# Kernel tuning notes

Measured on AMD Instinct MI355X. Metric: run time of the kernel, lower is better.

The kernel has to match this reference:

```python
import jax, jax.numpy as jnp
import numpy as np

BATCH = 64
IN_VECN = 1024
IN_VECL = 64
OUT_VECN = 64
OUT_VECL = 32
ROUTINGS = 3
EPS = 1e-5


def squash(x, axis=-1, eps=EPS):
    # squash(x) = |x|^2/(1+|x|^2) * x/(|x|+eps), matching the torch source
    n = jnp.linalg.norm(x, axis=axis, keepdims=True)
    n2 = n * n
    return n2 / (1.0 + n2) * x / (n + eps)


def setup_inputs() -> dict:
    key = jax.random.key(0)
    k1, k2, k3 = jax.random.split(key, 3)
    stdv = 1.0 / np.sqrt(IN_VECN * IN_VECL)  # reset_parameters: uniform(-stdv, stdv)
    u = jax.random.normal(k1, (BATCH, IN_VECN, IN_VECL), dtype=jnp.float32)
    weight = jax.random.uniform(k2, (IN_VECN, OUT_VECN, OUT_VECL, IN_VECL),
                                dtype=jnp.float32, minval=-stdv, maxval=stdv)
    bias = jax.random.uniform(k3, (IN_VECN, OUT_VECN, OUT_VECL),
                              dtype=jnp.float32, minval=-stdv, maxval=stdv)
    return {"u": u, "weight": weight, "bias": bias}


def reference(u, weight, bias):
    # u: [B, N, I]; weight: [N, O, L, I]; bias: [N, O, L]
    # u_hat: [B, N, O, L] -- per-input-capsule prediction for each output capsule
    u_hat = jnp.einsum('bni,noli->bnol', u, weight) + bias[None]
    # retain_grad=False: routing uses detached u_hat
    ud = jax.lax.stop_gradient(u_hat)
    # initial c = softmax(zeros) over out_vecn -> uniform 1/O, shape [1,1,O,1]
    c = jnp.full((1, 1, OUT_VECN, 1), 1.0 / OUT_VECN, dtype=u.dtype)
    b = jnp.zeros((u.shape[0], IN_VECN, OUT_VECN, 1), dtype=u.dtype)
    for _ in range(ROUTINGS - 1):
        v = squash(jnp.sum(ud * c, axis=-3), axis=-1)        # [B, O, L]
        b = b + jnp.sum(ud * v[:, None], axis=-1, keepdims=True)  # [B, N, O, 1]
        c = jax.nn.softmax(b, axis=-2)                        # softmax over O
    return squash(jnp.sum(u_hat * c, axis=-3), axis=-1)      # [B, O, L]
```

## Files before the change

### kernel.cpp

```cpp
#include <hip/hip_runtime.h>

#define BATCH 64
#define NIN 1024
#define IVL 64
#define ONUM 64
#define LVL 32
#define OLSZ 2048

typedef __attribute__((ext_vector_type(4))) float f32x4;
typedef __attribute__((ext_vector_type(8))) short short8;

#define STR_(x) #x
#define STR(x) STR_(x)

static __device__ __forceinline__ unsigned short f2bf(float f) {
  unsigned u = __builtin_bit_cast(unsigned, f);
  u += 0x7fffu + ((u >> 16) & 1u);
  return (unsigned short)(u >> 16);
}
static __device__ __forceinline__ float bf2f_lo(unsigned x) {
  return __builtin_bit_cast(float, x << 16);
}
static __device__ __forceinline__ float bf2f_hi(unsigned x) {
  return __builtin_bit_cast(float, x & 0xffff0000u);
}

#define W_BURST8(W, q0, q1)                                              \
  asm volatile(                                                          \
      "global_load_dwordx4 %[w0], %[a0], off\n\t"                        \
      "global_load_dwordx4 %[w1], %[a0], off offset:16\n\t"              \
      "global_load_dwordx4 %[w2], %[a0], off offset:128\n\t"             \
      "global_load_dwordx4 %[w3], %[a0], off offset:144\n\t"             \
      "global_load_dwordx4 %[w4], %[a1], off\n\t"                        \
      "global_load_dwordx4 %[w5], %[a1], off offset:16\n\t"              \
      "global_load_dwordx4 %[w6], %[a1], off offset:128\n\t"             \
      "global_load_dwordx4 %[w7], %[a1], off offset:144\n\t"             \
      : [w0] "=&v"(W[0]), [w1] "=&v"(W[1]), [w2] "=&v"(W[2]),            \
        [w3] "=&v"(W[3]), [w4] "=&v"(W[4]), [w5] "=&v"(W[5]),            \
        [w6] "=&v"(W[6]), [w7] "=&v"(W[7])                               \
      : [a0] "v"(q0), [a1] "v"(q1)                                       \
      : "memory")

#define VM_WAIT8                                        \
  do {                                                  \
    asm volatile("s_waitcnt vmcnt(8)" ::: "memory");    \
    __builtin_amdgcn_sched_barrier(0);                  \
  } while (0)
#define VM_WAIT0                                        \
  do {                                                  \
    asm volatile("s_waitcnt vmcnt(0)" ::: "memory");    \
    __builtin_amdgcn_sched_barrier(0);                  \
  } while (0)

#define STEP(W, C, O0, O1)                                                    \
  do {                                                                        \
    uint2 pks[8];                                                             \
    _Pragma("unroll") for (int tile = 0; tile < 2; ++tile) {                  \
      const f32x4 A0 = W[tile * 4 + 0];                                       \
      const f32x4 A1 = W[tile * 4 + 1];                                       \
      const f32x4 A2 = W[tile * 4 + 2];                                       \
      const f32x4 A3 = W[tile * 4 + 3];                                       \
      short8 wf0, wf1;                                                        \
      wf0[0] = (short)f2bf(A0[0]); wf0[1] = (short)f2bf(A0[1]);               \
      wf0[2] = (short)f2bf(A0[2]); wf0[3] = (short)f2bf(A0[3]);               \
      wf0[4] = (short)f2bf(A1[0]); wf0[5] = (short)f2bf(A1[1]);               \
      wf0[6] = (short)f2bf(A1[2]); wf0[7] = (short)f2bf(A1[3]);               \
      wf1[0] = (short)f2bf(A2[0]); wf1[1] = (short)f2bf(A2[1]);               \
      wf1[2] = (short)f2bf(A2[2]); wf1[3] = (short)f2bf(A2[3]);               \
      wf1[4] = (short)f2bf(A3[0]); wf1[5] = (short)f2bf(A3[1]);               \
      wf1[6] = (short)f2bf(A3[2]); wf1[7] = (short)f2bf(A3[3]);               \
      float4 bf = *(const float4*)&bias_lds[wave * 256 + (C)*32 + tile * 16 + \
                                            quad * 4];                        \
      f32x4 acc0 = (f32x4){0.f, 0.f, 0.f, 0.f};                               \
      f32x4 acc1 = acc0, acc2 = acc0, acc3 = acc0;                            \
      acc0 = __builtin_amdgcn_mfma_f32_16x16x32_bf16(wf0, uf[0][0], acc0, 0, 0, 0); \
      acc0 = __builtin_amdgcn_mfma_f32_16x16x32_bf16(wf1, uf[0][1], acc0, 0, 0, 0); \
      acc1 = __builtin_amdgcn_mfma_f32_16x16x32_bf16(wf0, uf[1][0], acc1, 0, 0, 0); \
      acc1 = __builtin_amdgcn_mfma_f32_16x16x32_bf16(wf1, uf[1][1], acc1, 0, 0, 0); \
      acc2 = __builtin_amdgcn_mfma_f32_16x16x32_bf16(wf0, uf[2][0], acc2, 0, 0, 0); \
      acc2 = __builtin_amdgcn_mfma_f32_16x16x32_bf16(wf1, uf[2][1], acc2, 0, 0, 0); \
      acc3 = __builtin_amdgcn_mfma_f32_16x16x32_bf16(wf0, uf[3][0], acc3, 0, 0, 0); \
      acc3 = __builtin_amdgcn_mfma_f32_16x16x32_bf16(wf1, uf[3][1], acc3, 0, 0, 0); \
      pks[0 * 2 + tile] = make_uint2(                                         \
          f2bf(acc0[0] + bf.x) | (f2bf(acc0[1] + bf.y) << 16),                \
          f2bf(acc0[2] + bf.z) | (f2bf(acc0[3] + bf.w) << 16));               \
      pks[1 * 2 + tile] = make_uint2(                                         \
          f2bf(acc1[0] + bf.x) | (f2bf(acc1[1] + bf.y) << 16),                \
          f2bf(acc1[2] + bf.z) | (f2bf(acc1[3] + bf.w) << 16));               \
      pks[2 * 2 + tile] = make_uint2(                                         \
          f2bf(acc2[0] + bf.x) | (f2bf(acc2[1] + bf.y) << 16),                \
          f2bf(acc2[2] + bf.z) | (f2bf(acc2[3] + bf.w) << 16));               \
      pks[3 * 2 + tile] = make_uint2(                                         \
          f2bf(acc3[0] + bf.x) | (f2bf(acc3[1] + bf.y) << 16),                \
          f2bf(acc3[2] + bf.z) | (f2bf(acc3[3] + bf.w) << 16));               \
    }                                                                         \
    asm volatile(                                                             \
        "global_store_dwordx2 %[a0], %[d0], off offset:" STR(O0) "\n\t"       \
        "global_store_dwordx2 %[a0], %[d1], off offset:" STR(O1) "\n\t"       \
        "global_store_dwordx2 %[a1], %[d2], off offset:" STR(O0) "\n\t"       \
        "global_store_dwordx2 %[a1], %[d3], off offset:" STR(O1) "\n\t"       \
        "global_store_dwordx2 %[a2], %[d4], off offset:" STR(O0) "\n\t"       \
        "global_store_dwordx2 %[a2], %[d5], off offset:" STR(O1) "\n\t"       \
        "global_store_dwordx2 %[a3], %[d6], off offset:" STR(O0) "\n\t"       \
        "global_store_dwordx2 %[a3], %[d7], off offset:" STR(O1) "\n\t"       \
        :: [a0] "v"(sb0), [a1] "v"(sb1), [a2] "v"(sb2), [a3] "v"(sb3),        \
           [d0] "v"(pks[0]), [d1] "v"(pks[1]), [d2] "v"(pks[2]),              \
           [d3] "v"(pks[3]), [d4] "v"(pks[4]), [d5] "v"(pks[5]),              \
           [d6] "v"(pks[6]), [d7] "v"(pks[7])                                 \
        : "memory");                                                          \
  } while (0)

__global__ __launch_bounds__(256, 3) void k_gemm(
    const float* __restrict__ u, const float* __restrict__ w,
    const float* __restrict__ bias, unsigned short* __restrict__ uhat,
    float* __restrict__ szero) {
  const int n = blockIdx.x;
  const int half = blockIdx.y;
  __shared__ __align__(16) unsigned short a_lds[64 * 72];
  __shared__ __align__(16) float bias_lds[1024];
  const int t = threadIdx.x;
  const int lane = t & 63;
  const int wave = t >> 6;
  const int row16 = lane & 15;
  const int quad = lane >> 4;

  {
    const int bid = blockIdx.y * gridDim.x + blockIdx.x;
    if (t < 192) szero[bid * 192 + t] = 0.f;
  }

  {
    const int b = t >> 2;
    const int i0 = (t & 3) * 16;
    const float* src = u + (size_t)b * (NIN * IVL) + (size_t)n * IVL + i0;
    unsigned short* dst = a_lds + b * 72 + i0;
#pragma unroll
    for (int q = 0; q < 4; ++q) {
      float4 v = *(const float4*)(src + q * 4);
      dst[q * 4 + 0] = f2bf(v.x);
      dst[q * 4 + 1] = f2bf(v.y);
      dst[q * 4 + 2] = f2bf(v.z);
      dst[q * 4 + 3] = f2bf(v.w);
    }
    *(float4*)&bias_lds[t * 4] =
        *(const float4*)(bias + (size_t)n * OLSZ + half * 1024 + t * 4);
  }

  const float* wp = w + (size_t)n * (OLSZ * IVL) +
                    (size_t)(half * 1024 + wave * 256 + row16) * IVL + quad * 8;
  f32x4 bufA[8], bufB[8];
  W_BURST8(bufA, wp, wp + 1024);
  W_BURST8(bufB, wp + 2048, wp + 3072);

  asm volatile("s_waitcnt lgkmcnt(0)" ::: "memory");
  __builtin_amdgcn_s_barrier();

  short8 uf[4][2];
#pragma unroll
  for (int bt = 0; bt < 4; ++bt) {
#pragma unroll
    for (int ks = 0; ks < 2; ++ks) {
      uf[bt][ks] =
          *(const short8*)(a_lds + (bt * 16 + row16) * 72 + ks * 32 + quad * 8);
    }
  }

  const unsigned short* sb0 = uhat + ((size_t)row16 * NIN + n) * OLSZ +
                              half * 1024 + wave * 256 + quad * 4;
  const unsigned short* sb1 = sb0 + (size_t)16 * NIN * OLSZ;
  const unsigned short* sb2 = sb0 + (size_t)32 * NIN * OLSZ;
  const unsigned short* sb3 = sb0 + (size_t)48 * NIN * OLSZ;

  VM_WAIT8; STEP(bufA, 0, 0, 32);    W_BURST8(bufA, wp + 4096,  wp + 5120);
  VM_WAIT8; STEP(bufB, 1, 64, 96);   W_BURST8(bufB, wp + 6144,  wp + 7168);
  VM_WAIT8; STEP(bufA, 2, 128, 160); W_BURST8(bufA, wp + 8192,  wp + 9216);
  VM_WAIT8; STEP(bufB, 3, 192, 224); W_BURST8(bufB, wp + 10240, wp + 11264);
  VM_WAIT8; STEP(bufA, 4, 256, 288); W_BURST8(bufA, wp + 12288, wp + 13312);
  VM_WAIT8; STEP(bufB, 5, 320, 352); W_BURST8(bufB, wp + 14336, wp + 15360);
  VM_WAIT8; STEP(bufA, 6, 384, 416);
  VM_WAIT0; STEP(bufB, 7, 448, 480);
}

__global__ __launch_bounds__(256) void k_sum_n(
    const unsigned short* __restrict__ uhat, float* __restrict__ s1) {
  const int b = blockIdx.x >> 5;
  const int chunk = blockIdx.x & 31;
  const int t = threadIdx.x;
  const unsigned short* base =
      uhat + ((size_t)b * NIN + (size_t)chunk * 32) * OLSZ + t * 8;
  float acc[8];
#pragma unroll
  for (int j = 0; j < 8; ++j) acc[j] = 0.f;
#pragma unroll 4
  for (int k = 0; k < 32; ++k) {
    uint4 p = *(const uint4*)(base + (size_t)k * OLSZ);
    unsigned xs[4] = {p.x, p.y, p.z, p.w};
#pragma unroll
    for (int h = 0; h < 4; ++h) {
      acc[2 * h] += bf2f_lo(xs[h]);
      acc[2 * h + 1] += bf2f_hi(xs[h]);
    }
  }
  float* s = s1 + (size_t)b * OLSZ + t * 8;
#pragma unroll
  for (int j = 0; j < 8; ++j) atomicAdd(s + j, acc[j]);
}

__global__ __launch_bounds__(256) void k_route(
    const unsigned short* __restrict__ uhat, const float* __restrict__ sv,
    float scale, float* __restrict__ b1, int add_b1,
    float* __restrict__ sout) {
  const int b = blockIdx.x >> 5;
  const int chunk = blockIdx.x & 31;
  const int t = threadIdx.x;
  const int lane = t & 63;
  const int wave = t >> 6;
  const int g = lane >> 2;
  __shared__ float red[4][OLSZ];

  float v[4][8];
#pragma unroll
  for (int q = 0; q < 4; ++q) {
    const float* svp = sv + (size_t)b * OLSZ + q * 512 + lane * 8;
    float4 a0 = *(const float4*)svp;
    float4 a1 = *(const float4*)(svp + 4);
    v[q][0] = a0.x * scale; v[q][1] = a0.y * scale;
    v[q][2] = a0.z * scale; v[q][3] = a0.w * scale;
    v[q][4] = a1.x * scale; v[q][5] = a1.y * scale;
    v[q][6] = a1.z * scale; v[q][7] = a1.w * scale;
    float p = 0.f;
#pragma unroll
    for (int j = 0; j < 8; ++j) p = fmaf(v[q][j], v[q][j], p);
    p += __shfl_xor(p, 1);
    p += __shfl_xor(p, 2);
    float f = p / ((1.f + p) * (sqrtf(p) + 1e-5f));
#pragma unroll
    for (int j = 0; j < 8; ++j) v[q][j] *= f;
  }

  float racc[4][8];
#pragma unroll
  for (int q = 0; q < 4; ++q)
#pragma unroll
    for (int j = 0; j < 8; ++j) racc[q][j] = 0.f;

  const int n0 = chunk * 32 + wave * 8;
  const unsigned short* ub = uhat + ((size_t)b * NIN + n0) * OLSZ + lane * 8;

  uint4 pA[4], pB[4];
#pragma unroll
  for (int q = 0; q < 4; ++q) pA[q] = *(const uint4*)(ub + q * 512);

  auto process = [&](const uint4(&pk)[4], int k) {
    const int n = n0 + k;
    const size_t bbase = ((size_t)b * NIN + n) * ONUM + g;
    float b1v[4];
    if (add_b1) {
#pragma unroll
      for (int q = 0; q < 4; ++q) b1v[q] = b1[bbase + 16 * q];
    }
    float ud[4][8];
    float d[4];
#pragma unroll
    for (int q = 0; q < 4; ++q) {
      unsigned xs[4] = {pk[q].x, pk[q].y, pk[q].z, pk[q].w};
#pragma unroll
      for (int h = 0; h < 4; ++h) {
        ud[q][2 * h] = bf2f_lo(xs[h]);
        ud[q][2 * h + 1] = bf2f_hi(xs[h]);
      }
      float p = 0.f;
#pragma unroll
      for (int j = 0; j < 8; ++j) p = fmaf(ud[q][j], v[q][j], p);
      p += __shfl_xor(p, 1);
      p += __shfl_xor(p, 2);
      d[q] = p;
    }
    float bno[4];
    if (add_b1) {
#pragma unroll
      for (int q = 0; q < 4; ++q) bno[q] = d[q] + b1v[q];
    } else {
#pragma unroll
      for (int q = 0; q < 4; ++q) bno[q] = d[q];
      if ((lane & 3) == 0) {
#pragma unroll
        for (int q = 0; q < 4; ++q) b1[bbase + 16 * q] = d[q];
      }
    }
    float m = fmaxf(fmaxf(bno[0], bno[1]), fmaxf(bno[2], bno[3]));
#pragma unroll
    for (int dl = 4; dl < 64; dl <<= 1) m = fmaxf(m, __shfl_xor(m, dl));
    float e0 = __expf(bno[0] - m);
    float e1 = __expf(bno[1] - m);
    float e2 = __expf(bno[2] - m);
    float e3 = __expf(bno[3] - m);
    float ls = (e0 + e1) + (e2 + e3);
#pragma unroll
    for (int dl = 4; dl < 64; dl <<= 1) ls += __shfl_xor(ls, dl);
    float inv = 1.0f / ls;
    float c[4] = {e0 * inv, e1 * inv, e2 * inv, e3 * inv};
#pragma unroll
    for (int q = 0; q < 4; ++q) {
#pragma unroll
      for (int j = 0; j < 8; ++j)
        racc[q][j] = fmaf(c[q], ud[q][j], racc[q][j]);
    }
  };

#pragma unroll
  for (int kk = 0; kk < 4; ++kk) {
    {
#pragma unroll
      for (int q = 0; q < 4; ++q)
        pB[q] = *(const uint4*)(ub + (size_t)(2 * kk + 1) * OLSZ + q * 512);
    }
    process(pA, 2 * kk);
    if (2 * kk + 2 < 8) {
#pragma unroll
      for (int q = 0; q < 4; ++q)
        pA[q] = *(const uint4*)(ub + (size_t)(2 * kk + 2) * OLSZ + q * 512);
    }
    process(pB, 2 * kk + 1);
  }

#pragma unroll
  for (int q = 0; q < 4; ++q) {
    float* dst = &red[wave][q * 512 + lane * 8];
    *(float4*)(dst) =
        make_float4(racc[q][0], racc[q][1], racc[q][2], racc[q][3]);
    *(float4*)(dst + 4) =
        make_float4(racc[q][4], racc[q][5], racc[q][6], racc[q][7]);
  }
  __syncthreads();
  float* so = sout + (size_t)b * OLSZ;
#pragma unroll
  for (int j = 0; j < 8; ++j) {
    const int idx = t + 256 * j;
    float s = (red[0][idx] + red[1][idx]) + (red[2][idx] + red[3][idx]);
    atomicAdd(so + idx, s);
  }
}

__global__ __launch_bounds__(256) void k_final(const float* __restrict__ s3,
                                               float* __restrict__ out) {
  const int b = blockIdx.x;
  const int t = threadIdx.x;
  __shared__ float norm2[64];
  if (t < 64) norm2[t] = 0.f;
  __syncthreads();
  float scv[8];
#pragma unroll
  for (int k = 0; k < 8; ++k) {
    int idx = t + k * 256;
    float sc = s3[b * OLSZ + idx];
    scv[k] = sc;
    atomicAdd(&norm2[idx >> 5], sc * sc);
  }
  __syncthreads();
#pragma unroll
  for (int k = 0; k < 8; ++k) {
    int idx = t + k * 256;
    int o = idx >> 5;
    float n2 = norm2[o];
    float f = n2 / ((1.f + n2) * (sqrtf(n2) + 1e-5f));
    out[b * OLSZ + idx] = scv[k] * f;
  }
}

extern "C" void kernel_launch(void* const* d_in, const int* in_sizes, int n_in,
                              void* d_out, int out_size, void* d_ws,
                              size_t ws_size, hipStream_t stream) {
  const float* u = (const float*)d_in[0];
  const float* w = (const float*)d_in[1];
  const float* bias = (const float*)d_in[2];
  float* out = (float*)d_out;

  char* ws = (char*)d_ws;
  unsigned short* uhat = (unsigned short*)ws;
  float* b1 = (float*)(ws + (size_t)268435456);
  float* s1 = (float*)(ws + (size_t)268435456 + 16777216);
  float* s2 = s1 + 131072;
  float* s3 = s2 + 131072;

  k_gemm<<<dim3(1024, 2), dim3(256), 0, stream>>>(u, w, bias, uhat, s1);
  k_sum_n<<<dim3(2048), dim3(256), 0, stream>>>(uhat, s1);
  k_route<<<dim3(2048), dim3(256), 0, stream>>>(uhat, s1, 1.0f / 64.0f, b1, 0, s2);
  k_route<<<dim3(2048), dim3(256), 0, stream>>>(uhat, s2, 1.0f, b1, 1, s3);
  k_final<<<dim3(64), dim3(256), 0, stream>>>(s3, out);
}
```

Before: 529.0 us.

## Permute uhat layout for 32-byte stores and deepen weight load bursts

The GEMM kernel now writes each lane's bf16 outputs as contiguous 32-byte chunks with dwordx4 stores, replacing strided dwordx2 stores. It also loads weights in 16-load bursts over 4 steps instead of 8-load bursts over 8 steps, and lowers the occupancy hint from 3 to 2 blocks per CU to make room for the larger register buffers. The permuted uhat layout is undone in the routing kernel through new lane-to-capsule index maps and shuffle patterns, and in the final kernel through index remapping on output. The risks are lower occupancy and subtle indexing errors in the permutation.

```diff
diff --git a/kernel.cpp b/kernel.cpp
--- a/kernel.cpp
+++ b/kernel.cpp
@@ -1,6 +1,5 @@
 #include <hip/hip_runtime.h>
 
-#define BATCH 64
 #define NIN 1024
 #define IVL 64
 #define ONUM 64
@@ -8,10 +7,8 @@
 #define OLSZ 2048
 
 typedef __attribute__((ext_vector_type(4))) float f32x4;
+typedef __attribute__((ext_vector_type(4))) unsigned u32x4;
 typedef __attribute__((ext_vector_type(8))) short short8;
-
-#define STR_(x) #x
-#define STR(x) STR_(x)
 
 static __device__ __forceinline__ unsigned short f2bf(float f) {
   unsigned u = __builtin_bit_cast(unsigned, f);
@@ -25,7 +22,7 @@
   return __builtin_bit_cast(float, x & 0xffff0000u);
 }
 
-#define W_BURST8(W, q0, q1)                                              \
+#define W_BURST16(W, q0, q1, q2, q3)                                     \
   asm volatile(                                                          \
       "global_load_dwordx4 %[w0], %[a0], off\n\t"                        \
       "global_load_dwordx4 %[w1], %[a0], off offset:16\n\t"              \
@@ -35,82 +32,98 @@
       "global_load_dwordx4 %[w5], %[a1], off offset:16\n\t"              \
       "global_load_dwordx4 %[w6], %[a1], off offset:128\n\t"             \
       "global_load_dwordx4 %[w7], %[a1], off offset:144\n\t"             \
+      "global_load_dwordx4 %[w8], %[a2], off\n\t"                        \
+      "global_load_dwordx4 %[w9], %[a2], off offset:16\n\t"              \
+      "global_load_dwordx4 %[w10], %[a2], off offset:128\n\t"            \
+      "global_load_dwordx4 %[w11], %[a2], off offset:144\n\t"            \
+      "global_load_dwordx4 %[w12], %[a3], off\n\t"                       \
+      "global_load_dwordx4 %[w13], %[a3], off offset:16\n\t"             \
+      "global_load_dwordx4 %[w14], %[a3], off offset:128\n\t"            \
+      "global_load_dwordx4 %[w15], %[a3], off offset:144\n\t"            \
       : [w0] "=&v"(W[0]), [w1] "=&v"(W[1]), [w2] "=&v"(W[2]),            \
         [w3] "=&v"(W[3]), [w4] "=&v"(W[4]), [w5] "=&v"(W[5]),            \
-        [w6] "=&v"(W[6]), [w7] "=&v"(W[7])                               \
-      : [a0] "v"(q0), [a1] "v"(q1)                                       \
+        [w6] "=&v"(W[6]), [w7] "=&v"(W[7]), [w8] "=&v"(W[8]),            \
+        [w9] "=&v"(W[9]), [w10] "=&v"(W[10]), [w11] "=&v"(W[11]),        \
+        [w12] "=&v"(W[12]), [w13] "=&v"(W[13]), [w14] "=&v"(W[14]),      \
+        [w15] "=&v"(W[15])                                               \
+      : [a0] "v"(q0), [a1] "v"(q1), [a2] "v"(q2), [a3] "v"(q3)           \
       : "memory")
 
+#define VM_WAIT16                                       \
+  do {                                                  \
+    asm volatile("s_waitcnt vmcnt(16)" ::: "memory");   \
+    __builtin_amdgcn_sched_barrier(0);                  \
+  } while (0)
 #define VM_WAIT8                                        \
   do {                                                  \
     asm volatile("s_waitcnt vmcnt(8)" ::: "memory");    \
     __builtin_amdgcn_sched_barrier(0);                  \
   } while (0)
-#define VM_WAIT0                                        \
-  do {                                                  \
-    asm volatile("s_waitcnt vmcnt(0)" ::: "memory");    \
-    __builtin_amdgcn_sched_barrier(0);                  \
+
+#define TILE(W, TL, C, O0, O1, O2, O3, O4, O5, O6, O7)                        \
+  do {                                                                        \
+    const f32x4 A0 = (W)[(TL) * 4 + 0];                                       \
+    const f32x4 A1 = (W)[(TL) * 4 + 1];                                       \
+    const f32x4 A2 = (W)[(TL) * 4 + 2];                                       \
+    const f32x4 A3 = (W)[(TL) * 4 + 3];                                       \
+    short8 wf0, wf1;                                                          \
+    wf0[0] = (short)f2bf(A0[0]); wf0[1] = (short)f2bf(A0[1]);                 \
+    wf0[2] = (short)f2bf(A0[2]); wf0[3] = (short)f2bf(A0[3]);                 \
+    wf0[4] = (short)f2bf(A1[0]); wf0[5] = (short)f2bf(A1[1]);                 \
+    wf0[6] = (short)f2bf(A1[2]); wf0[7] = (short)f2bf(A1[3]);                 \
+    wf1[0] = (short)f2bf(A2[0]); wf1[1] = (short)f2bf(A2[1]);                 \
+    wf1[2] = (short)f2bf(A2[2]); wf1[3] = (short)f2bf(A2[3]);                 \
+    wf1[4] = (short)f2bf(A3[0]); wf1[5] = (short)f2bf(A3[1]);                 \
+    wf1[6] = (short)f2bf(A3[2]); wf1[7] = (short)f2bf(A3[3]);                 \
+    float4 bf = *(const float4*)&bias_lds[wave * 256 + (C) * 64 + (TL) * 16 + \
+                                          quad * 4];                          \
+    f32x4 a0 = (f32x4){0.f, 0.f, 0.f, 0.f};                                   \
+    f32x4 a1 = a0, a2 = a0, a3 = a0;                                          \
+    a0 = __builtin_amdgcn_mfma_f32_16x16x32_bf16(wf0, uf[0][0], a0, 0, 0, 0); \
+    a0 = __builtin_amdgcn_mfma_f32_16x16x32_bf16(wf1, uf[0][1], a0, 0, 0, 0); \
+    a1 = __builtin_amdgcn_mfma_f32_16x16x32_bf16(wf0, uf[1][0], a1, 0, 0, 0); \
+    a1 = __builtin_amdgcn_mfma_f32_16x16x32_bf16(wf1, uf[1][1], a1, 0, 0, 0); \
+    a2 = __builtin_amdgcn_mfma_f32_16x16x32_bf16(wf0, uf[2][0], a2, 0, 0, 0); \
+    a2 = __builtin_amdgcn_mfma_f32_16x16x32_bf16(wf1, uf[2][1], a2, 0, 0, 0); \
+    a3 = __builtin_amdgcn_mfma_f32_16x16x32_bf16(wf0, uf[3][0], a3, 0, 0, 0); \
+    a3 = __builtin_amdgcn_mfma_f32_16x16x32_bf16(wf1, uf[3][1], a3, 0, 0, 0); \
+    O0 = f2bf(a0[0] + bf.x) | ((unsigned)f2bf(a0[1] + bf.y) << 16);           \
+    O1 = f2bf(a0[2] + bf.z) | ((unsigned)f2bf(a0[3] + bf.w) << 16);           \
+    O2 = f2bf(a1[0] + bf.x) | ((unsigned)f2bf(a1[1] + bf.y) << 16);           \
+    O3 = f2bf(a1[2] + bf.z) | ((unsigned)f2bf(a1[3] + bf.w) << 16);           \
+    O4 = f2bf(a2[0] + bf.x) | ((unsigned)f2bf(a2[1] + bf.y) << 16);           \
+    O5 = f2bf(a2[2] + bf.z) | ((unsigned)f2bf(a2[3] + bf.w) << 16);           \
+    O6 = f2bf(a3[0] + bf.x) | ((unsigned)f2bf(a3[1] + bf.y) << 16);           \
+    O7 = f2bf(a3[2] + bf.z) | ((unsigned)f2bf(a3[3] + bf.w) << 16);           \
   } while (0)
 
-#define STEP(W, C, O0, O1)                                                    \
+#define STEP(W, C)                                                            \
   do {                                                                        \
-    uint2 pks[8];                                                             \
-    _Pragma("unroll") for (int tile = 0; tile < 2; ++tile) {                  \
-      const f32x4 A0 = W[tile * 4 + 0];                                       \
-      const f32x4 A1 = W[tile * 4 + 1];                                       \
-      const f32x4 A2 = W[tile * 4 + 2];                                       \
-      const f32x4 A3 = W[tile * 4 + 3];                                       \
-      short8 wf0, wf1;                                                        \
-      wf0[0] = (short)f2bf(A0[0]); wf0[1] = (short)f2bf(A0[1]);               \
-      wf0[2] = (short)f2bf(A0[2]); wf0[3] = (short)f2bf(A0[3]);               \
-      wf0[4] = (short)f2bf(A1[0]); wf0[5] = (short)f2bf(A1[1]);               \
-      wf0[6] = (short)f2bf(A1[2]); wf0[7] = (short)f2bf(A1[3]);               \
-      wf1[0] = (short)f2bf(A2[0]); wf1[1] = (short)f2bf(A2[1]);               \
-      wf1[2] = (short)f2bf(A2[2]); wf1[3] = (short)f2bf(A2[3]);               \
-      wf1[4] = (short)f2bf(A3[0]); wf1[5] = (short)f2bf(A3[1]);               \
-      wf1[6] = (short)f2bf(A3[2]); wf1[7] = (short)f2bf(A3[3]);               \
-      float4 bf = *(const float4*)&bias_lds[wave * 256 + (C)*32 + tile * 16 + \
-                                            quad * 4];                        \
-      f32x4 acc0 = (f32x4){0.f, 0.f, 0.f, 0.f};                               \
-      f32x4 acc1 = acc0, acc2 = acc0, acc3 = acc0;                            \
-      acc0 = __builtin_amdgcn_mfma_f32_16x16x32_bf16(wf0, uf[0][0], acc0, 0, 0, 0); \
-      acc0 = __builtin_amdgcn_mfma_f32_16x16x32_bf16(wf1, uf[0][1], acc0, 0, 0, 0); \
-      acc1 = __builtin_amdgcn_mfma_f32_16x16x32_bf16(wf0, uf[1][0], acc1, 0, 0, 0); \
-      acc1 = __builtin_amdgcn_mfma_f32_16x16x32_bf16(wf1, uf[1][1], acc1, 0, 0, 0); \
-      acc2 = __builtin_amdgcn_mfma_f32_16x16x32_bf16(wf0, uf[2][0], acc2, 0, 0, 0); \
-      acc2 = __builtin_amdgcn_mfma_f32_16x16x32_bf16(wf1, uf[2][1], acc2, 0, 0, 0); \
-      acc3 = __builtin_amdgcn_mfma_f32_16x16x32_bf16(wf0, uf[3][0], acc3, 0, 0, 0); \
-      acc3 = __builtin_amdgcn_mfma_f32_16x16x32_bf16(wf1, uf[3][1], acc3, 0, 0, 0); \
-      pks[0 * 2 + tile] = make_uint2(                                         \
-          f2bf(acc0[0] + bf.x) | (f2bf(acc0[1] + bf.y) << 16),                \
-          f2bf(acc0[2] + bf.z) | (f2bf(acc0[3] + bf.w) << 16));               \
-      pks[1 * 2 + tile] = make_uint2(                                         \
-          f2bf(acc1[0] + bf.x) | (f2bf(acc1[1] + bf.y) << 16),                \
-          f2bf(acc1[2] + bf.z) | (f2bf(acc1[3] + bf.w) << 16));               \
-      pks[2 * 2 + tile] = make_uint2(                                         \
-          f2bf(acc2[0] + bf.x) | (f2bf(acc2[1] + bf.y) << 16),                \
-          f2bf(acc2[2] + bf.z) | (f2bf(acc2[3] + bf.w) << 16));               \
-      pks[3 * 2 + tile] = make_uint2(                                         \
-          f2bf(acc3[0] + bf.x) | (f2bf(acc3[1] + bf.y) << 16),                \
-          f2bf(acc3[2] + bf.z) | (f2bf(acc3[3] + bf.w) << 16));               \
-    }                                                                         \
+    u32x4 kA0, kA1, kA2, kA3, kB0, kB1, kB2, kB3;                             \
+    TILE(W, 0, C, kA0.x, kA0.y, kA1.x, kA1.y, kA2.x, kA2.y, kA3.x, kA3.y);    \
+    TILE(W, 1, C, kA0.z, kA0.w, kA1.z, kA1.w, kA2.z, kA2.w, kA3.z, kA3.w);    \
+    TILE(W, 2, C, kB0.x, kB0.y, kB1.x, kB1.y, kB2.x, kB2.y, kB3.x, kB3.y);    \
+    TILE(W, 3, C, kB0.z, kB0.w, kB1.z, kB1.w, kB2.z, kB2.w, kB3.z, kB3.w);    \
+    const unsigned short* c0 = sb0 + (C) * 64;                                \
+    const unsigned short* c1 = sb1 + (C) * 64;                                \
+    const unsigned short* c2 = sb2 + (C) * 64;                                \
+    const unsigned short* c3 = sb3 + (C) * 64;                                \
     asm volatile(                                                             \
-        "global_store_dwordx2 %[a0], %[d0], off offset:" STR(O0) "\n\t"       \
-        "global_store_dwordx2 %[a0], %[d1], off offset:" STR(O1) "\n\t"       \
-        "global_store_dwordx2 %[a1], %[d2], off offset:" STR(O0) "\n\t"       \
-        "global_store_dwordx2 %[a1], %[d3], off offset:" STR(O1) "\n\t"       \
-        "global_store_dwordx2 %[a2], %[d4], off offset:" STR(O0) "\n\t"       \
-        "global_store_dwordx2 %[a2], %[d5], off offset:" STR(O1) "\n\t"       \
-        "global_store_dwordx2 %[a3], %[d6], off offset:" STR(O0) "\n\t"       \
-        "global_store_dwordx2 %[a3], %[d7], off offset:" STR(O1) "\n\t"       \
-        :: [a0] "v"(sb0), [a1] "v"(sb1), [a2] "v"(sb2), [a3] "v"(sb3),        \
-           [d0] "v"(pks[0]), [d1] "v"(pks[1]), [d2] "v"(pks[2]),              \
-           [d3] "v"(pks[3]), [d4] "v"(pks[4]), [d5] "v"(pks[5]),              \
-           [d6] "v"(pks[6]), [d7] "v"(pks[7])                                 \
+        "global_store_dwordx4 %[a0], %[d0], off\n\t"                          \
+        "global_store_dwordx4 %[a0], %[d1], off offset:16\n\t"                \
+        "global_store_dwordx4 %[a1], %[d2], off\n\t"                          \
+        "global_store_dwordx4 %[a1], %[d3], off offset:16\n\t"                \
+        "global_store_dwordx4 %[a2], %[d4], off\n\t"                          \
+        "global_store_dwordx4 %[a2], %[d5], off offset:16\n\t"                \
+        "global_store_dwordx4 %[a3], %[d6], off\n\t"                          \
+        "global_store_dwordx4 %[a3], %[d7], off offset:16\n\t"                \
+        :: [a0] "v"(c0), [a1] "v"(c1), [a2] "v"(c2), [a3] "v"(c3),            \
+           [d0] "v"(kA0), [d1] "v"(kB0), [d2] "v"(kA1), [d3] "v"(kB1),        \
+           [d4] "v"(kA2), [d5] "v"(kB2), [d6] "v"(kA3), [d7] "v"(kB3)         \
         : "memory");                                                          \
   } while (0)
 
-__global__ __launch_bounds__(256, 3) void k_gemm(
+__global__ __launch_bounds__(256, 2) void k_gemm(
     const float* __restrict__ u, const float* __restrict__ w,
     const float* __restrict__ bias, unsigned short* __restrict__ uhat,
     float* __restrict__ szero) {
@@ -125,7 +138,7 @@
   const int quad = lane >> 4;
 
   {
-    const int bid = blockIdx.y * gridDim.x + blockIdx.x;
+    const int bid = half * 1024 + n;
     if (t < 192) szero[bid * 192 + t] = 0.f;
   }
 
@@ -148,9 +161,9 @@
 
   const float* wp = w + (size_t)n * (OLSZ * IVL) +
                     (size_t)(half * 1024 + wave * 256 + row16) * IVL + quad * 8;
-  f32x4 bufA[8], bufB[8];
-  W_BURST8(bufA, wp, wp + 1024);
-  W_BURST8(bufB, wp + 2048, wp + 3072);
+  f32x4 bufA[16], bufB[16];
+  W_BURST16(bufA, wp, wp + 1024, wp + 2048, wp + 3072);
+  W_BURST16(bufB, wp + 4096, wp + 5120, wp + 6144, wp + 7168);
 
   asm volatile("s_waitcnt lgkmcnt(0)" ::: "memory");
   __builtin_amdgcn_s_barrier();
@@ -166,19 +179,15 @@
   }
 
   const unsigned short* sb0 = uhat + ((size_t)row16 * NIN + n) * OLSZ +
-                              half * 1024 + wave * 256 + quad * 4;
+                              half * 1024 + wave * 256 + quad * 16;
   const unsigned short* sb1 = sb0 + (size_t)16 * NIN * OLSZ;
   const unsigned short* sb2 = sb0 + (size_t)32 * NIN * OLSZ;
   const unsigned short* sb3 = sb0 + (size_t)48 * NIN * OLSZ;
 
-  VM_WAIT8; STEP(bufA, 0, 0, 32);    W_BURST8(bufA, wp + 4096,  wp + 5120);
-  VM_WAIT8; STEP(bufB, 1, 64, 96);   W_BURST8(bufB, wp + 6144,  wp + 7168);
-  VM_WAIT8; STEP(bufA, 2, 128, 160); W_BURST8(bufA, wp + 8192,  wp + 9216);
-  VM_WAIT8; STEP(bufB, 3, 192, 224); W_BURST8(bufB, wp + 10240, wp + 11264);
-  VM_WAIT8; STEP(bufA, 4, 256, 288); W_BURST8(bufA, wp + 12288, wp + 13312);
-  VM_WAIT8; STEP(bufB, 5, 320, 352); W_BURST8(bufB, wp + 14336, wp + 15360);
-  VM_WAIT8; STEP(bufA, 6, 384, 416);
-  VM_WAIT0; STEP(bufB, 7, 448, 480);
+  VM_WAIT16; STEP(bufA, 0); W_BURST16(bufA, wp + 8192, wp + 9216, wp + 10240, wp + 11264);
+  VM_WAIT16; STEP(bufB, 1); W_BURST16(bufB, wp + 12288, wp + 13312, wp + 14336, wp + 15360);
+  VM_WAIT16; STEP(bufA, 2);
+  VM_WAIT8;  STEP(bufB, 3);
 }
 
 __global__ __launch_bounds__(256) void k_sum_n(
@@ -215,7 +224,7 @@
   const int t = threadIdx.x;
   const int lane = t & 63;
   const int wave = t >> 6;
-  const int g = lane >> 2;
+  const int g2 = ((lane >> 3) << 1) | (lane & 1);
   __shared__ float red[4][OLSZ];
 
   float v[4][8];
@@ -231,8 +240,8 @@
     float p = 0.f;
 #pragma unroll
     for (int j = 0; j < 8; ++j) p = fmaf(v[q][j], v[q][j], p);
-    p += __shfl_xor(p, 1);
     p += __shfl_xor(p, 2);
+    p += __shfl_xor(p, 4);
     float f = p / ((1.f + p) * (sqrtf(p) + 1e-5f));
 #pragma unroll
     for (int j = 0; j < 8; ++j) v[q][j] *= f;
@@ -253,7 +262,7 @@
 
   auto process = [&](const uint4(&pk)[4], int k) {
     const int n = n0 + k;
-    const size_t bbase = ((size_t)b * NIN + n) * ONUM + g;
+    const size_t bbase = ((size_t)b * NIN + n) * ONUM + g2;
     float b1v[4];
     if (add_b1) {
 #pragma unroll
@@ -272,8 +281,8 @@
       float p = 0.f;
 #pragma unroll
       for (int j = 0; j < 8; ++j) p = fmaf(ud[q][j], v[q][j], p);
-      p += __shfl_xor(p, 1);
       p += __shfl_xor(p, 2);
+      p += __shfl_xor(p, 4);
       d[q] = p;
     }
     float bno[4];
@@ -283,21 +292,25 @@
     } else {
 #pragma unroll
       for (int q = 0; q < 4; ++q) bno[q] = d[q];
-      if ((lane & 3) == 0) {
+      if ((lane & 6) == 0) {
 #pragma unroll
         for (int q = 0; q < 4; ++q) b1[bbase + 16 * q] = d[q];
       }
     }
     float m = fmaxf(fmaxf(bno[0], bno[1]), fmaxf(bno[2], bno[3]));
-#pragma unroll
-    for (int dl = 4; dl < 64; dl <<= 1) m = fmaxf(m, __shfl_xor(m, dl));
+    m = fmaxf(m, __shfl_xor(m, 1));
+    m = fmaxf(m, __shfl_xor(m, 8));
+    m = fmaxf(m, __shfl_xor(m, 16));
+    m = fmaxf(m, __shfl_xor(m, 32));
     float e0 = __expf(bno[0] - m);
     float e1 = __expf(bno[1] - m);
     float e2 = __expf(bno[2] - m);
     float e3 = __expf(bno[3] - m);
     float ls = (e0 + e1) + (e2 + e3);
-#pragma unroll
-    for (int dl = 4; dl < 64; dl <<= 1) ls += __shfl_xor(ls, dl);
+    ls += __shfl_xor(ls, 1);
+    ls += __shfl_xor(ls, 8);
+    ls += __shfl_xor(ls, 16);
+    ls += __shfl_xor(ls, 32);
     float inv = 1.0f / ls;
     float c[4] = {e0 * inv, e1 * inv, e2 * inv, e3 * inv};
 #pragma unroll
@@ -355,16 +368,21 @@
     int idx = t + k * 256;
     float sc = s3[b * OLSZ + idx];
     scv[k] = sc;
-    atomicAdd(&norm2[idx >> 5], sc * sc);
+    int o = ((idx >> 9) << 4) + (((idx >> 6) & 7) << 1) + ((idx >> 3) & 1);
+    atomicAdd(&norm2[o], sc * sc);
   }
   __syncthreads();
 #pragma unroll
   for (int k = 0; k < 8; ++k) {
     int idx = t + k * 256;
-    int o = idx >> 5;
+    int o = ((idx >> 9) << 4) + (((idx >> 6) & 7) << 1) + ((idx >> 3) & 1);
     float n2 = norm2[o];
     float f = n2 / ((1.f + n2) * (sqrtf(n2) + 1e-5f));
-    out[b * OLSZ + idx] = scv[k] * f;
+    int q2 = (idx >> 4) & 3;
+    int t2 = (idx >> 2) & 3;
+    int j = idx & 3;
+    int fr = (idx & ~63) | (t2 << 4) | (q2 << 2) | j;
+    out[b * OLSZ + fr] = scv[k] * f;
   }
 }
 
```

Measured after the change: 479.6 us. -9.3%, faster.
